# Performance work log

Measured on AMD Instinct MI355X. Metric: run time of the kernel, lower is better.

The kernel has to match this reference:

```python
import jax, jax.numpy as jnp
import numpy as np

B, S, D, V = 2, 2048, 1024, 32000
EPSILON = 5.0


def setup_inputs() -> dict:
    key = jax.random.key(0)
    k1, k2, k3, k4 = jax.random.split(key, 4)
    inputs_embeds = jax.random.normal(k1, (B, S, D), dtype=jnp.float32)
    table = jax.random.normal(k2, (V, D), dtype=jnp.float32)
    # dx-privacy noise: unit-norm Gaussian direction * Gamma(alpha=D, rate=eps*D) scalar sample
    noise_v = jax.random.normal(k3, (B, S, D), dtype=jnp.float32)
    norm = jnp.linalg.norm(noise_v, axis=-1, keepdims=True)
    norm = jnp.where(norm > 0, norm, jnp.ones_like(norm))
    gamma_scale = jax.random.gamma(k4, jnp.float32(D)) / jnp.float32(EPSILON * D)
    noise = gamma_scale * (noise_v / norm)
    return {"inputs_embeds": inputs_embeds, "table": table, "noise": noise}


def reference(inputs_embeds, table, noise):
    # perturb embeddings with precomputed dx-privacy noise (no_grad in original)
    perturbed = inputs_embeds + noise                      # [B,S,D]
    # full similarity matrix vs vocabulary, then nearest-embedding snap
    sims = jnp.einsum('bsd,vd->bsv', perturbed, table)     # [B,S,V]
    max_token = jnp.argmax(sims, axis=-1)                  # [B,S] int
    res = jnp.take(table, max_token, axis=0)               # [B,S,D]
    return res
```

## Files before the change

### kernel.cpp

```cpp
#include <hip/hip_runtime.h>
#include <stdint.h>

#define ROWS 4096
#define DIM 1024
#define VOCAB 32000
#define BM 128
#define BN 128
#define NTILES (VOCAB / BN)
#define NCHUNKS 24
#define SCALE 2048.0f

typedef float floatx4 __attribute__((ext_vector_type(4)));
typedef _Float16 f16x8 __attribute__((ext_vector_type(8)));
typedef _Float16 f16x4 __attribute__((ext_vector_type(4)));

__device__ __forceinline__ void load_lds16(const _Float16* g, _Float16* l) {
    __builtin_amdgcn_global_load_lds(
        (const __attribute__((address_space(1))) uint32_t*)g,
        (__attribute__((address_space(3))) uint32_t*)l, 16, 0, 0);
}

__global__ void init_keys(unsigned long long* __restrict__ keys) {
    int i = blockIdx.x * 256 + threadIdx.x;
    if (i < ROWS) keys[i] = 0ull;
}

__global__ void prep(const float* __restrict__ emb, const float* __restrict__ noi,
                     const float* __restrict__ table,
                     _Float16* __restrict__ Ah, _Float16* __restrict__ Al,
                     _Float16* __restrict__ Bh, _Float16* __restrict__ Bl,
                     unsigned long long* __restrict__ keys) {
    const int bid = blockIdx.x;
    const int ABLK = ROWS * DIM / 8 / 256;
    if (bid < ABLK) {
        if (bid < ROWS / 256) keys[bid * 256 + threadIdx.x] = 0ull;
        size_t i = ((size_t)bid * 256 + threadIdx.x) * 8;
        floatx4 a = *(const floatx4*)(emb + i);
        floatx4 b = *(const floatx4*)(emb + i + 4);
        floatx4 c = *(const floatx4*)(noi + i);
        floatx4 d = *(const floatx4*)(noi + i + 4);
        f16x8 h, l;
#pragma unroll
        for (int j = 0; j < 4; j++) {
            float p = (a[j] + c[j]) * SCALE;
            _Float16 hh = (_Float16)p;
            h[j] = hh; l[j] = (_Float16)(p - (float)hh);
            float q = (b[j] + d[j]) * SCALE;
            _Float16 hq = (_Float16)q;
            h[4 + j] = hq; l[4 + j] = (_Float16)(q - (float)hq);
        }
        *(f16x8*)(Ah + i) = h;
        *(f16x8*)(Al + i) = l;
    } else {
        size_t i = ((size_t)(bid - ABLK) * 256 + threadIdx.x) * 8;
        floatx4 a = *(const floatx4*)(table + i);
        floatx4 b = *(const floatx4*)(table + i + 4);
        f16x8 h, l;
#pragma unroll
        for (int j = 0; j < 4; j++) {
            float p = a[j] * SCALE;
            _Float16 hh = (_Float16)p;
            h[j] = hh; l[j] = (_Float16)(p - (float)hh);
            float q = b[j] * SCALE;
            _Float16 hq = (_Float16)q;
            h[4 + j] = hq; l[4 + j] = (_Float16)(q - (float)hq);
        }
        *(f16x8*)(Bh + i) = h;
        *(f16x8*)(Bl + i) = l;
    }
}

__global__ __launch_bounds__(256, 3) void gemm_argmax_pre(
    const _Float16* __restrict__ Ah, const _Float16* __restrict__ Al,
    const _Float16* __restrict__ Bh, const _Float16* __restrict__ Bl,
    unsigned long long* __restrict__ keys) {
    __shared__ __align__(16) _Float16 sAh[BM * 32];
    __shared__ __align__(16) _Float16 sAl[BM * 32];
    __shared__ __align__(16) _Float16 sBh[BN * 32];
    __shared__ __align__(16) _Float16 sBl[BN * 32];
    __shared__ unsigned long long redk[BM];

    const int tid = threadIdx.x;
    const int w = tid >> 6, lane = tid & 63;
    const int quad = lane >> 4, lq = lane & 15;
    const int rb = blockIdx.x / NCHUNKS, chunk = blockIdx.x % NCHUNKS;
    const int row0 = rb * BM;
    const int wmb = (w & 1) * 4, wnb = (w >> 1) * 4;
    const int wm = wmb * 16, wn = wnb * 16;
    const int tstart = chunk * NTILES / NCHUNKS;
    const int tend = (chunk + 1) * NTILES / NCHUNKS;

    if (tid < BM) redk[tid] = 0ull;

    union PF { f16x8 v; _Float16 s[8]; } fidx, fone;
#pragma unroll
    for (int j = 0; j < 8; j++) { fidx.s[j] = (_Float16)0.0f; fone.s[j] = (_Float16)0.0f; }
    if (quad == 0) { fidx.s[0] = (_Float16)(float)lq; fone.s[0] = (_Float16)1.0f; }
    floatx4 c1 = {0.f, 0.f, 0.f, 0.f}, c2 = {0.f, 0.f, 0.f, 0.f};
    c1 = __builtin_amdgcn_mfma_f32_16x16x32_f16(fidx.v, fone.v, c1, 0, 0, 0);
    c2 = __builtin_amdgcn_mfma_f32_16x16x32_f16(fone.v, fidx.v, c2, 0, 0, 0);
    int m_of[4], n_of[4];
#pragma unroll
    for (int r = 0; r < 4; r++) {
        m_of[r] = (int)(c1[r] + 0.5f);
        n_of[r] = (int)(c2[r] + 0.5f);
    }

    const _Float16* gbase = (w == 0) ? (Ah + (size_t)row0 * DIM)
                        : (w == 1) ? (Al + (size_t)row0 * DIM)
                        : (w == 2) ? Bh : Bl;
    _Float16* ldst = (w == 0) ? sAh : (w == 1) ? sAl : (w == 2) ? sBh : sBl;
    const int piece = (lane & 3) ^ ((lane >> 3) & 3);
    const size_t g_lane = (size_t)(lane >> 2) * DIM + (size_t)piece * 8;
    const int rdo = lq * 32 + (quad ^ ((lq >> 1) & 3)) * 8;
    const bool isB = (w >= 2);

    float rmax[16];
    int ridx[16];
#pragma unroll
    for (int i = 0; i < 16; i++) { rmax[i] = -3.4e38f; ridx[i] = 0; }

    for (int t = tstart; t < tend; ++t) {
        const int n0 = t * BN;
        const _Float16* gsrc = gbase + (isB ? (size_t)t * BN * DIM : 0) + g_lane;
        floatx4 acc[4][4];
#pragma unroll
        for (int mi = 0; mi < 4; mi++)
#pragma unroll
            for (int ni = 0; ni < 4; ni++)
#pragma unroll
                for (int r = 0; r < 4; r++) acc[mi][ni][r] = 0.0f;

        for (int kt = 0; kt < DIM / 32; ++kt) {
            const int k0 = kt * 32;
            __syncthreads();
#pragma unroll
            for (int c = 0; c < 8; c++)
                load_lds16(gsrc + (size_t)(c * 16) * DIM + k0, ldst + c * 512);
            __syncthreads();

            f16x8 ahf[4], alf[4];
#pragma unroll
            for (int i = 0; i < 4; i++) {
                ahf[i] = *(const f16x8*)(&sAh[(wmb + i) * 512 + rdo]);
                alf[i] = *(const f16x8*)(&sAl[(wmb + i) * 512 + rdo]);
            }
#pragma unroll
            for (int ni = 0; ni < 4; ni++) {
                f16x8 bh = *(const f16x8*)(&sBh[(wnb + ni) * 512 + rdo]);
                f16x8 bl = *(const f16x8*)(&sBl[(wnb + ni) * 512 + rdo]);
#pragma unroll
                for (int mi = 0; mi < 4; mi++) {
                    acc[mi][ni] = __builtin_amdgcn_mfma_f32_16x16x32_f16(
                        ahf[mi], bh, acc[mi][ni], 0, 0, 0);
                    acc[mi][ni] = __builtin_amdgcn_mfma_f32_16x16x32_f16(
                        ahf[mi], bl, acc[mi][ni], 0, 0, 0);
                    acc[mi][ni] = __builtin_amdgcn_mfma_f32_16x16x32_f16(
                        alf[mi], bh, acc[mi][ni], 0, 0, 0);
                }
            }
        }
#pragma unroll
        for (int mi = 0; mi < 4; mi++)
#pragma unroll
            for (int ni = 0; ni < 4; ni++)
#pragma unroll
                for (int r = 0; r < 4; r++) {
                    float v = acc[mi][ni][r];
                    int col = n0 + wn + ni * 16 + n_of[r];
                    int s = mi * 4 + r;
                    if (v > rmax[s] || (v == rmax[s] && col < ridx[s])) {
                        rmax[s] = v;
                        ridx[s] = col;
                    }
                }
    }

#pragma unroll
    for (int s = 0; s < 16; ++s) {
        int mi = s >> 2, r = s & 3;
        int rowl = wm + mi * 16 + m_of[r];
        union { float f; uint32_t i; } u;
        u.f = rmax[s];
        uint32_t ord = (u.i & 0x80000000u) ? ~u.i : (u.i | 0x80000000u);
        unsigned long long key =
            ((unsigned long long)ord << 32) | (uint32_t)(~(uint32_t)ridx[s]);
        atomicMax(&redk[rowl], key);
    }
    __syncthreads();
    if (tid < BM) atomicMax(&keys[row0 + tid], redk[tid]);
}

#define BKF 64
#define LDKF 72
#define TILES_PER_WGF 10
#define NCHUNKSF 25

__global__ __launch_bounds__(256, 2) void gemm_argmax_fused(
    const float* __restrict__ emb, const float* __restrict__ noi,
    const float* __restrict__ table, unsigned long long* __restrict__ keys) {
    __shared__ __align__(16) _Float16 Ah[BM * LDKF];
    __shared__ __align__(16) _Float16 Al[BM * LDKF];
    __shared__ __align__(16) _Float16 Bh[BN * LDKF];
    __shared__ __align__(16) _Float16 Bl[BN * LDKF];
    __shared__ unsigned long long redk[BM];

    const int tid = threadIdx.x;
    const int wave = tid >> 6, lane = tid & 63;
    const int quad = lane >> 4, lq = lane & 15;
    const int rb = blockIdx.x / NCHUNKSF, chunk = blockIdx.x % NCHUNKSF;
    const int row0 = rb * BM;
    const int wm = (wave & 1) * 64, wn = (wave >> 1) * 64;

    if (tid < BM) redk[tid] = 0ull;

    union PF { f16x8 v; _Float16 s[8]; } fidx, fone;
#pragma unroll
    for (int j = 0; j < 8; j++) { fidx.s[j] = (_Float16)0.0f; fone.s[j] = (_Float16)0.0f; }
    if (quad == 0) { fidx.s[0] = (_Float16)(float)lq; fone.s[0] = (_Float16)1.0f; }
    floatx4 c1 = {0.f, 0.f, 0.f, 0.f}, c2 = {0.f, 0.f, 0.f, 0.f};
    c1 = __builtin_amdgcn_mfma_f32_16x16x32_f16(fidx.v, fone.v, c1, 0, 0, 0);
    c2 = __builtin_amdgcn_mfma_f32_16x16x32_f16(fone.v, fidx.v, c2, 0, 0, 0);
    int m_of[4], n_of[4];
#pragma unroll
    for (int r = 0; r < 4; r++) {
        m_of[r] = (int)(c1[r] + 0.5f);
        n_of[r] = (int)(c2[r] + 0.5f);
    }

    float rmax[16];
    int ridx[16];
#pragma unroll
    for (int i = 0; i < 16; i++) { rmax[i] = -3.4e38f; ridx[i] = 0; }

    for (int t = 0; t < TILES_PER_WGF; ++t) {
        const int n0 = (chunk * TILES_PER_WGF + t) * BN;
        floatx4 acc[4][4];
#pragma unroll
        for (int mi = 0; mi < 4; mi++)
#pragma unroll
            for (int ni = 0; ni < 4; ni++)
#pragma unroll
                for (int r = 0; r < 4; r++) acc[mi][ni][r] = 0.0f;

        for (int kt = 0; kt < DIM / BKF; ++kt) {
            const int k0 = kt * BKF;
            __syncthreads();
#pragma unroll
            for (int i = 0; i < 8; i++) {
                int c = i * 256 + tid;
                int r = c >> 4, q = c & 15;
                floatx4 e = *(const floatx4*)(emb + (size_t)(row0 + r) * DIM + k0 + q * 4);
                floatx4 n = *(const floatx4*)(noi + (size_t)(row0 + r) * DIM + k0 + q * 4);
                floatx4 b = *(const floatx4*)(table + (size_t)(n0 + r) * DIM + k0 + q * 4);
                f16x4 ah, al, bh, bl;
#pragma unroll
                for (int j = 0; j < 4; j++) {
                    float pa = (e[j] + n[j]) * SCALE;
                    _Float16 h = (_Float16)pa;
                    ah[j] = h;
                    al[j] = (_Float16)(pa - (float)h);
                    float pb = b[j] * SCALE;
                    _Float16 hb = (_Float16)pb;
                    bh[j] = hb;
                    bl[j] = (_Float16)(pb - (float)hb);
                }
                *(f16x4*)(Ah + r * LDKF + q * 4) = ah;
                *(f16x4*)(Al + r * LDKF + q * 4) = al;
                *(f16x4*)(Bh + r * LDKF + q * 4) = bh;
                *(f16x4*)(Bl + r * LDKF + q * 4) = bl;
            }
            __syncthreads();
#pragma unroll
            for (int ks = 0; ks < BKF; ks += 32) {
                f16x8 bhf[4], blf[4], ahf[4], alf[4];
#pragma unroll
                for (int i = 0; i < 4; i++) {
                    bhf[i] = *(const f16x8*)(Bh + (wn + i * 16 + lq) * LDKF + ks + quad * 8);
                    blf[i] = *(const f16x8*)(Bl + (wn + i * 16 + lq) * LDKF + ks + quad * 8);
                    ahf[i] = *(const f16x8*)(Ah + (wm + i * 16 + lq) * LDKF + ks + quad * 8);
                    alf[i] = *(const f16x8*)(Al + (wm + i * 16 + lq) * LDKF + ks + quad * 8);
                }
#pragma unroll
                for (int mi = 0; mi < 4; mi++)
#pragma unroll
                    for (int ni = 0; ni < 4; ni++) {
                        acc[mi][ni] = __builtin_amdgcn_mfma_f32_16x16x32_f16(
                            ahf[mi], bhf[ni], acc[mi][ni], 0, 0, 0);
                        acc[mi][ni] = __builtin_amdgcn_mfma_f32_16x16x32_f16(
                            ahf[mi], blf[ni], acc[mi][ni], 0, 0, 0);
                        acc[mi][ni] = __builtin_amdgcn_mfma_f32_16x16x32_f16(
                            alf[mi], bhf[ni], acc[mi][ni], 0, 0, 0);
                    }
            }
        }
#pragma unroll
        for (int mi = 0; mi < 4; mi++)
#pragma unroll
            for (int ni = 0; ni < 4; ni++)
#pragma unroll
                for (int r = 0; r < 4; r++) {
                    float v = acc[mi][ni][r];
                    int col = n0 + wn + ni * 16 + n_of[r];
                    int s = mi * 4 + r;
                    if (v > rmax[s] || (v == rmax[s] && col < ridx[s])) {
                        rmax[s] = v;
                        ridx[s] = col;
                    }
                }
    }

#pragma unroll
    for (int s = 0; s < 16; ++s) {
        int mi = s >> 2, r = s & 3;
        int rowl = wm + mi * 16 + m_of[r];
        union { float f; uint32_t i; } u;
        u.f = rmax[s];
        uint32_t ord = (u.i & 0x80000000u) ? ~u.i : (u.i | 0x80000000u);
        unsigned long long key =
            ((unsigned long long)ord << 32) | (uint32_t)(~(uint32_t)ridx[s]);
        atomicMax(&redk[rowl], key);
    }
    __syncthreads();
    if (tid < BM) atomicMax(&keys[row0 + tid], redk[tid]);
}

__global__ void gather_kernel(const unsigned long long* __restrict__ keys,
                              const float* __restrict__ table,
                              float* __restrict__ out) {
    int row = blockIdx.x;
    unsigned long long key = keys[row];
    uint32_t ix = ~(uint32_t)(key & 0xFFFFFFFFull);
    const floatx4* src = (const floatx4*)(table + (size_t)ix * DIM);
    floatx4* dst = (floatx4*)(out + (size_t)row * DIM);
    dst[threadIdx.x] = src[threadIdx.x];
}

extern "C" void kernel_launch(void* const* d_in, const int* in_sizes, int n_in,
                              void* d_out, int out_size, void* d_ws, size_t ws_size,
                              hipStream_t stream) {
    (void)in_sizes; (void)n_in; (void)out_size;
    const float* emb = (const float*)d_in[0];
    const float* table = (const float*)d_in[1];
    const float* noi = (const float*)d_in[2];
    float* out = (float*)d_out;

    uint8_t* ws = (uint8_t*)d_ws;
    unsigned long long* keys = (unsigned long long*)ws;
    const size_t keysB = (size_t)ROWS * 8;
    const size_t aB = (size_t)ROWS * DIM * 2;
    const size_t bB = (size_t)VOCAB * DIM * 2;
    const size_t need = keysB + 2 * aB + 2 * bB;

    if (ws_size >= need) {
        _Float16* Ah = (_Float16*)(ws + keysB);
        _Float16* Al = (_Float16*)(ws + keysB + aB);
        _Float16* Bh = (_Float16*)(ws + keysB + 2 * aB);
        _Float16* Bl = (_Float16*)(ws + keysB + 2 * aB + bB);
        const int ablk = ROWS * DIM / 8 / 256;
        const int bblk = VOCAB * DIM / 8 / 256;
        prep<<<ablk + bblk, 256, 0, stream>>>(emb, noi, table, Ah, Al, Bh, Bl, keys);
        gemm_argmax_pre<<<(ROWS / BM) * NCHUNKS, 256, 0, stream>>>(Ah, Al, Bh, Bl, keys);
    } else {
        init_keys<<<ROWS / 256, 256, 0, stream>>>(keys);
        gemm_argmax_fused<<<(ROWS / BM) * NCHUNKSF, 256, 0, stream>>>(emb, noi, table, keys);
    }
    gather_kernel<<<ROWS, 256, 0, stream>>>(keys, table, out);
}
```

Measured before the change: 1.044 ms.

## Shrink pre-split GEMM tiles to 64x64 and double-buffer LDS loads

```diff
diff --git a/kernel.cpp b/kernel.cpp
--- a/kernel.cpp
+++ b/kernel.cpp
@@ -6,8 +6,10 @@
 #define VOCAB 32000
 #define BM 128
 #define BN 128
-#define NTILES (VOCAB / BN)
-#define NCHUNKS 24
+#define BMP 64
+#define BNP 64
+#define NTILESP (VOCAB / BNP)
+#define NCHUNKSP 12
 #define SCALE 2048.0f
 
 typedef float floatx4 __attribute__((ext_vector_type(4)));
@@ -74,23 +76,23 @@
     const _Float16* __restrict__ Ah, const _Float16* __restrict__ Al,
     const _Float16* __restrict__ Bh, const _Float16* __restrict__ Bl,
     unsigned long long* __restrict__ keys) {
-    __shared__ __align__(16) _Float16 sAh[BM * 32];
-    __shared__ __align__(16) _Float16 sAl[BM * 32];
-    __shared__ __align__(16) _Float16 sBh[BN * 32];
-    __shared__ __align__(16) _Float16 sBl[BN * 32];
-    __shared__ unsigned long long redk[BM];
+    __shared__ __align__(16) _Float16 sAh[2][BMP * 32];
+    __shared__ __align__(16) _Float16 sAl[2][BMP * 32];
+    __shared__ __align__(16) _Float16 sBh[2][BNP * 32];
+    __shared__ __align__(16) _Float16 sBl[2][BNP * 32];
+    __shared__ unsigned long long redk[BMP];
 
     const int tid = threadIdx.x;
     const int w = tid >> 6, lane = tid & 63;
     const int quad = lane >> 4, lq = lane & 15;
-    const int rb = blockIdx.x / NCHUNKS, chunk = blockIdx.x % NCHUNKS;
-    const int row0 = rb * BM;
-    const int wmb = (w & 1) * 4, wnb = (w >> 1) * 4;
+    const int rb = blockIdx.x / NCHUNKSP, chunk = blockIdx.x % NCHUNKSP;
+    const int row0 = rb * BMP;
+    const int wmb = (w & 1) * 2, wnb = (w >> 1) * 2;
     const int wm = wmb * 16, wn = wnb * 16;
-    const int tstart = chunk * NTILES / NCHUNKS;
-    const int tend = (chunk + 1) * NTILES / NCHUNKS;
-
-    if (tid < BM) redk[tid] = 0ull;
+    const int tstart = chunk * NTILESP / NCHUNKSP;
+    const int tend = (chunk + 1) * NTILESP / NCHUNKSP;
+
+    if (tid < BMP) redk[tid] = 0ull;
 
     union PF { f16x8 v; _Float16 s[8]; } fidx, fone;
 #pragma unroll
@@ -109,48 +111,65 @@
     const _Float16* gbase = (w == 0) ? (Ah + (size_t)row0 * DIM)
                         : (w == 1) ? (Al + (size_t)row0 * DIM)
                         : (w == 2) ? Bh : Bl;
-    _Float16* ldst = (w == 0) ? sAh : (w == 1) ? sAl : (w == 2) ? sBh : sBl;
+    _Float16* lbase = (w == 0) ? &sAh[0][0] : (w == 1) ? &sAl[0][0]
+                    : (w == 2) ? &sBh[0][0] : &sBl[0][0];
     const int piece = (lane & 3) ^ ((lane >> 3) & 3);
     const size_t g_lane = (size_t)(lane >> 2) * DIM + (size_t)piece * 8;
     const int rdo = lq * 32 + (quad ^ ((lq >> 1) & 3)) * 8;
     const bool isB = (w >= 2);
 
-    float rmax[16];
-    int ridx[16];
-#pragma unroll
-    for (int i = 0; i < 16; i++) { rmax[i] = -3.4e38f; ridx[i] = 0; }
+    float rmax[8];
+    int ridx[8];
+#pragma unroll
+    for (int i = 0; i < 8; i++) { rmax[i] = -3.4e38f; ridx[i] = 0; }
+
+#define STAGE(buf, tt, kk)                                                     \
+    do {                                                                       \
+        const _Float16* gs_ = gbase + (isB ? (size_t)(tt) * BNP * DIM : 0)     \
+                              + (size_t)(kk) * 32 + g_lane;                    \
+        _Float16* ld_ = lbase + (buf) * (BMP * 32);                            \
+        _Pragma("unroll")                                                      \
+        for (int c_ = 0; c_ < 4; c_++)                                         \
+            load_lds16(gs_ + (size_t)(c_ * 16) * DIM, ld_ + c_ * 512);         \
+    } while (0)
+
+    int cur = 0;
+    STAGE(0, tstart, 0);
 
     for (int t = tstart; t < tend; ++t) {
-        const int n0 = t * BN;
-        const _Float16* gsrc = gbase + (isB ? (size_t)t * BN * DIM : 0) + g_lane;
-        floatx4 acc[4][4];
-#pragma unroll
-        for (int mi = 0; mi < 4; mi++)
-#pragma unroll
-            for (int ni = 0; ni < 4; ni++)
+        const int n0 = t * BNP;
+        floatx4 acc[2][2];
+#pragma unroll
+        for (int mi = 0; mi < 2; mi++)
+#pragma unroll
+            for (int ni = 0; ni < 2; ni++)
 #pragma unroll
                 for (int r = 0; r < 4; r++) acc[mi][ni][r] = 0.0f;
 
         for (int kt = 0; kt < DIM / 32; ++kt) {
-            const int k0 = kt * 32;
-            __syncthreads();
-#pragma unroll
-            for (int c = 0; c < 8; c++)
-                load_lds16(gsrc + (size_t)(c * 16) * DIM + k0, ldst + c * 512);
-            __syncthreads();
-
-            f16x8 ahf[4], alf[4];
-#pragma unroll
-            for (int i = 0; i < 4; i++) {
-                ahf[i] = *(const f16x8*)(&sAh[(wmb + i) * 512 + rdo]);
-                alf[i] = *(const f16x8*)(&sAl[(wmb + i) * 512 + rdo]);
-            }
-#pragma unroll
-            for (int ni = 0; ni < 4; ni++) {
-                f16x8 bh = *(const f16x8*)(&sBh[(wnb + ni) * 512 + rdo]);
-                f16x8 bl = *(const f16x8*)(&sBl[(wnb + ni) * 512 + rdo]);
-#pragma unroll
-                for (int mi = 0; mi < 4; mi++) {
+            int nt = t, nk = kt + 1;
+            if (nk == DIM / 32) { nk = 0; ++nt; }
+            if (nt < tend) {
+                STAGE(cur ^ 1, nt, nk);
+                asm volatile("s_waitcnt vmcnt(4)" ::: "memory");
+            } else {
+                asm volatile("s_waitcnt vmcnt(0)" ::: "memory");
+            }
+            __builtin_amdgcn_s_barrier();
+
+            __builtin_amdgcn_s_setprio(1);
+            f16x8 ahf[2], alf[2];
+#pragma unroll
+            for (int i = 0; i < 2; i++) {
+                ahf[i] = *(const f16x8*)(&sAh[cur][(wmb + i) * 512 + rdo]);
+                alf[i] = *(const f16x8*)(&sAl[cur][(wmb + i) * 512 + rdo]);
+            }
+#pragma unroll
+            for (int ni = 0; ni < 2; ni++) {
+                f16x8 bh = *(const f16x8*)(&sBh[cur][(wnb + ni) * 512 + rdo]);
+                f16x8 bl = *(const f16x8*)(&sBl[cur][(wnb + ni) * 512 + rdo]);
+#pragma unroll
+                for (int mi = 0; mi < 2; mi++) {
                     acc[mi][ni] = __builtin_amdgcn_mfma_f32_16x16x32_f16(
                         ahf[mi], bh, acc[mi][ni], 0, 0, 0);
                     acc[mi][ni] = __builtin_amdgcn_mfma_f32_16x16x32_f16(
@@ -158,6 +177,146 @@
                     acc[mi][ni] = __builtin_amdgcn_mfma_f32_16x16x32_f16(
                         alf[mi], bh, acc[mi][ni], 0, 0, 0);
                 }
+            }
+            __builtin_amdgcn_s_setprio(0);
+
+            asm volatile("s_waitcnt lgkmcnt(0)" ::: "memory");
+            __builtin_amdgcn_s_barrier();
+            cur ^= 1;
+        }
+#pragma unroll
+        for (int mi = 0; mi < 2; mi++)
+#pragma unroll
+            for (int ni = 0; ni < 2; ni++)
+#pragma unroll
+                for (int r = 0; r < 4; r++) {
+                    float v = acc[mi][ni][r];
+                    int col = n0 + wn + ni * 16 + n_of[r];
+                    int s = mi * 4 + r;
+                    if (v > rmax[s] || (v == rmax[s] && col < ridx[s])) {
+                        rmax[s] = v;
+                        ridx[s] = col;
+                    }
+                }
+    }
+#undef STAGE
+
+#pragma unroll
+    for (int s = 0; s < 8; ++s) {
+        int mi = s >> 2, r = s & 3;
+        int rowl = wm + mi * 16 + m_of[r];
+        union { float f; uint32_t i; } u;
+        u.f = rmax[s];
+        uint32_t ord = (u.i & 0x80000000u) ? ~u.i : (u.i | 0x80000000u);
+        unsigned long long key =
+            ((unsigned long long)ord << 32) | (uint32_t)(~(uint32_t)ridx[s]);
+        atomicMax(&redk[rowl], key);
+    }
+    __syncthreads();
+    if (tid < BMP) atomicMax(&keys[row0 + tid], redk[tid]);
+}
+
+#define BKF 64
+#define LDKF 72
+#define TILES_PER_WGF 10
+#define NCHUNKSF 25
+
+__global__ __launch_bounds__(256, 2) void gemm_argmax_fused(
+    const float* __restrict__ emb, const float* __restrict__ noi,
+    const float* __restrict__ table, unsigned long long* __restrict__ keys) {
+    __shared__ __align__(16) _Float16 Ah[BM * LDKF];
+    __shared__ __align__(16) _Float16 Al[BM * LDKF];
+    __shared__ __align__(16) _Float16 Bh[BN * LDKF];
+    __shared__ __align__(16) _Float16 Bl[BN * LDKF];
+    __shared__ unsigned long long redk[BM];
+
+    const int tid = threadIdx.x;
+    const int wave = tid >> 6, lane = tid & 63;
+    const int quad = lane >> 4, lq = lane & 15;
+    const int rb = blockIdx.x / NCHUNKSF, chunk = blockIdx.x % NCHUNKSF;
+    const int row0 = rb * BM;
+    const int wm = (wave & 1) * 64, wn = (wave >> 1) * 64;
+
+    if (tid < BM) redk[tid] = 0ull;
+
+    union PF { f16x8 v; _Float16 s[8]; } fidx, fone;
+#pragma unroll
+    for (int j = 0; j < 8; j++) { fidx.s[j] = (_Float16)0.0f; fone.s[j] = (_Float16)0.0f; }
+    if (quad == 0) { fidx.s[0] = (_Float16)(float)lq; fone.s[0] = (_Float16)1.0f; }
+    floatx4 c1 = {0.f, 0.f, 0.f, 0.f}, c2 = {0.f, 0.f, 0.f, 0.f};
+    c1 = __builtin_amdgcn_mfma_f32_16x16x32_f16(fidx.v, fone.v, c1, 0, 0, 0);
+    c2 = __builtin_amdgcn_mfma_f32_16x16x32_f16(fone.v, fidx.v, c2, 0, 0, 0);
+    int m_of[4], n_of[4];
+#pragma unroll
+    for (int r = 0; r < 4; r++) {
+        m_of[r] = (int)(c1[r] + 0.5f);
+        n_of[r] = (int)(c2[r] + 0.5f);
+    }
+
+    float rmax[16];
+    int ridx[16];
+#pragma unroll
+    for (int i = 0; i < 16; i++) { rmax[i] = -3.4e38f; ridx[i] = 0; }
+
+    for (int t = 0; t < TILES_PER_WGF; ++t) {
+        const int n0 = (chunk * TILES_PER_WGF + t) * BN;
+        floatx4 acc[4][4];
+#pragma unroll
+        for (int mi = 0; mi < 4; mi++)
+#pragma unroll
+            for (int ni = 0; ni < 4; ni++)
+#pragma unroll
+                for (int r = 0; r < 4; r++) acc[mi][ni][r] = 0.0f;
+
+        for (int kt = 0; kt < DIM / BKF; ++kt) {
+            const int k0 = kt * BKF;
+            __syncthreads();
+#pragma unroll
+            for (int i = 0; i < 8; i++) {
+                int c = i * 256 + tid;
+                int r = c >> 4, q = c & 15;
+                floatx4 e = *(const floatx4*)(emb + (size_t)(row0 + r) * DIM + k0 + q * 4);
+                floatx4 n = *(const floatx4*)(noi + (size_t)(row0 + r) * DIM + k0 + q * 4);
+                floatx4 b = *(const floatx4*)(table + (size_t)(n0 + r) * DIM + k0 + q * 4);
+                f16x4 ah, al, bh, bl;
+#pragma unroll
+                for (int j = 0; j < 4; j++) {
+                    float pa = (e[j] + n[j]) * SCALE;
+                    _Float16 h = (_Float16)pa;
+                    ah[j] = h;
+                    al[j] = (_Float16)(pa - (float)h);
+                    float pb = b[j] * SCALE;
+                    _Float16 hb = (_Float16)pb;
+                    bh[j] = hb;
+                    bl[j] = (_Float16)(pb - (float)hb);
+                }
+                *(f16x4*)(Ah + r * LDKF + q * 4) = ah;
+                *(f16x4*)(Al + r * LDKF + q * 4) = al;
+                *(f16x4*)(Bh + r * LDKF + q * 4) = bh;
+                *(f16x4*)(Bl + r * LDKF + q * 4) = bl;
+            }
+            __syncthreads();
+#pragma unroll
+            for (int ks = 0; ks < BKF; ks += 32) {
+                f16x8 bhf[4], blf[4], ahf[4], alf[4];
+#pragma unroll
+                for (int i = 0; i < 4; i++) {
+                    bhf[i] = *(const f16x8*)(Bh + (wn + i * 16 + lq) * LDKF + ks + quad * 8);
+                    blf[i] = *(const f16x8*)(Bl + (wn + i * 16 + lq) * LDKF + ks + quad * 8);
+                    ahf[i] = *(const f16x8*)(Ah + (wm + i * 16 + lq) * LDKF + ks + quad * 8);
+                    alf[i] = *(const f16x8*)(Al + (wm + i * 16 + lq) * LDKF + ks + quad * 8);
+                }
+#pragma unroll
+                for (int mi = 0; mi < 4; mi++)
+#pragma unroll
+                    for (int ni = 0; ni < 4; ni++) {
+                        acc[mi][ni] = __builtin_amdgcn_mfma_f32_16x16x32_f16(
+                            ahf[mi], bhf[ni], acc[mi][ni], 0, 0, 0);
+                        acc[mi][ni] = __builtin_amdgcn_mfma_f32_16x16x32_f16(
+                            ahf[mi], blf[ni], acc[mi][ni], 0, 0, 0);
+                        acc[mi][ni] = __builtin_amdgcn_mfma_f32_16x16x32_f16(
+                            alf[mi], bhf[ni], acc[mi][ni], 0, 0, 0);
+                    }
             }
         }
 #pragma unroll
@@ -191,140 +350,6 @@
     if (tid < BM) atomicMax(&keys[row0 + tid], redk[tid]);
 }
 
-#define BKF 64
-#define LDKF 72
-#define TILES_PER_WGF 10
-#define NCHUNKSF 25
-
-__global__ __launch_bounds__(256, 2) void gemm_argmax_fused(
-    const float* __restrict__ emb, const float* __restrict__ noi,
-    const float* __restrict__ table, unsigned long long* __restrict__ keys) {
-    __shared__ __align__(16) _Float16 Ah[BM * LDKF];
-    __shared__ __align__(16) _Float16 Al[BM * LDKF];
-    __shared__ __align__(16) _Float16 Bh[BN * LDKF];
-    __shared__ __align__(16) _Float16 Bl[BN * LDKF];
-    __shared__ unsigned long long redk[BM];
-
-    const int tid = threadIdx.x;
-    const int wave = tid >> 6, lane = tid & 63;
-    const int quad = lane >> 4, lq = lane & 15;
-    const int rb = blockIdx.x / NCHUNKSF, chunk = blockIdx.x % NCHUNKSF;
-    const int row0 = rb * BM;
-    const int wm = (wave & 1) * 64, wn = (wave >> 1) * 64;
-
-    if (tid < BM) redk[tid] = 0ull;
-
-    union PF { f16x8 v; _Float16 s[8]; } fidx, fone;
-#pragma unroll
-    for (int j = 0; j < 8; j++) { fidx.s[j] = (_Float16)0.0f; fone.s[j] = (_Float16)0.0f; }
-    if (quad == 0) { fidx.s[0] = (_Float16)(float)lq; fone.s[0] = (_Float16)1.0f; }
-    floatx4 c1 = {0.f, 0.f, 0.f, 0.f}, c2 = {0.f, 0.f, 0.f, 0.f};
-    c1 = __builtin_amdgcn_mfma_f32_16x16x32_f16(fidx.v, fone.v, c1, 0, 0, 0);
-    c2 = __builtin_amdgcn_mfma_f32_16x16x32_f16(fone.v, fidx.v, c2, 0, 0, 0);
-    int m_of[4], n_of[4];
-#pragma unroll
-    for (int r = 0; r < 4; r++) {
-        m_of[r] = (int)(c1[r] + 0.5f);
-        n_of[r] = (int)(c2[r] + 0.5f);
-    }
-
-    float rmax[16];
-    int ridx[16];
-#pragma unroll
-    for (int i = 0; i < 16; i++) { rmax[i] = -3.4e38f; ridx[i] = 0; }
-
-    for (int t = 0; t < TILES_PER_WGF; ++t) {
-        const int n0 = (chunk * TILES_PER_WGF + t) * BN;
-        floatx4 acc[4][4];
-#pragma unroll
-        for (int mi = 0; mi < 4; mi++)
-#pragma unroll
-            for (int ni = 0; ni < 4; ni++)
-#pragma unroll
-                for (int r = 0; r < 4; r++) acc[mi][ni][r] = 0.0f;
-
-        for (int kt = 0; kt < DIM / BKF; ++kt) {
-            const int k0 = kt * BKF;
-            __syncthreads();
-#pragma unroll
-            for (int i = 0; i < 8; i++) {
-                int c = i * 256 + tid;
-                int r = c >> 4, q = c & 15;
-                floatx4 e = *(const floatx4*)(emb + (size_t)(row0 + r) * DIM + k0 + q * 4);
-                floatx4 n = *(const floatx4*)(noi + (size_t)(row0 + r) * DIM + k0 + q * 4);
-                floatx4 b = *(const floatx4*)(table + (size_t)(n0 + r) * DIM + k0 + q * 4);
-                f16x4 ah, al, bh, bl;
-#pragma unroll
-                for (int j = 0; j < 4; j++) {
-                    float pa = (e[j] + n[j]) * SCALE;
-                    _Float16 h = (_Float16)pa;
-                    ah[j] = h;
-                    al[j] = (_Float16)(pa - (float)h);
-                    float pb = b[j] * SCALE;
-                    _Float16 hb = (_Float16)pb;
-                    bh[j] = hb;
-                    bl[j] = (_Float16)(pb - (float)hb);
-                }
-                *(f16x4*)(Ah + r * LDKF + q * 4) = ah;
-                *(f16x4*)(Al + r * LDKF + q * 4) = al;
-                *(f16x4*)(Bh + r * LDKF + q * 4) = bh;
-                *(f16x4*)(Bl + r * LDKF + q * 4) = bl;
-            }
-            __syncthreads();
-#pragma unroll
-            for (int ks = 0; ks < BKF; ks += 32) {
-                f16x8 bhf[4], blf[4], ahf[4], alf[4];
-#pragma unroll
-                for (int i = 0; i < 4; i++) {
-                    bhf[i] = *(const f16x8*)(Bh + (wn + i * 16 + lq) * LDKF + ks + quad * 8);
-                    blf[i] = *(const f16x8*)(Bl + (wn + i * 16 + lq) * LDKF + ks + quad * 8);
-                    ahf[i] = *(const f16x8*)(Ah + (wm + i * 16 + lq) * LDKF + ks + quad * 8);
-                    alf[i] = *(const f16x8*)(Al + (wm + i * 16 + lq) * LDKF + ks + quad * 8);
-                }
-#pragma unroll
-                for (int mi = 0; mi < 4; mi++)
-#pragma unroll
-                    for (int ni = 0; ni < 4; ni++) {
-                        acc[mi][ni] = __builtin_amdgcn_mfma_f32_16x16x32_f16(
-                            ahf[mi], bhf[ni], acc[mi][ni], 0, 0, 0);
-                        acc[mi][ni] = __builtin_amdgcn_mfma_f32_16x16x32_f16(
-                            ahf[mi], blf[ni], acc[mi][ni], 0, 0, 0);
-                        acc[mi][ni] = __builtin_amdgcn_mfma_f32_16x16x32_f16(
-                            alf[mi], bhf[ni], acc[mi][ni], 0, 0, 0);
-                    }
-            }
-        }
-#pragma unroll
-        for (int mi = 0; mi < 4; mi++)
-#pragma unroll
-            for (int ni = 0; ni < 4; ni++)
-#pragma unroll
-                for (int r = 0; r < 4; r++) {
-                    float v = acc[mi][ni][r];
-                    int col = n0 + wn + ni * 16 + n_of[r];
-                    int s = mi * 4 + r;
-                    if (v > rmax[s] || (v == rmax[s] && col < ridx[s])) {
-                        rmax[s] = v;
-                        ridx[s] = col;
-                    }
-                }
-    }
-
-#pragma unroll
-    for (int s = 0; s < 16; ++s) {
-        int mi = s >> 2, r = s & 3;
-        int rowl = wm + mi * 16 + m_of[r];
-        union { float f; uint32_t i; } u;
-        u.f = rmax[s];
-        uint32_t ord = (u.i & 0x80000000u) ? ~u.i : (u.i | 0x80000000u);
-        unsigned long long key =
-            ((unsigned long long)ord << 32) | (uint32_t)(~(uint32_t)ridx[s]);
-        atomicMax(&redk[rowl], key);
-    }
-    __syncthreads();
-    if (tid < BM) atomicMax(&keys[row0 + tid], redk[tid]);
-}
-
 __global__ void gather_kernel(const unsigned long long* __restrict__ keys,
                               const float* __restrict__ table,
                               float* __restrict__ out) {
@@ -360,7 +385,7 @@
         const int ablk = ROWS * DIM / 8 / 256;
         const int bblk = VOCAB * DIM / 8 / 256;
         prep<<<ablk + bblk, 256, 0, stream>>>(emb, noi, table, Ah, Al, Bh, Bl, keys);
-        gemm_argmax_pre<<<(ROWS / BM) * NCHUNKS, 256, 0, stream>>>(Ah, Al, Bh, Bl, keys);
+        gemm_argmax_pre<<<(ROWS / BMP) * NCHUNKSP, 256, 0, stream>>>(Ah, Al, Bh, Bl, keys);
     } else {
         init_keys<<<ROWS / 256, 256, 0, stream>>>(keys);
         gemm_argmax_fused<<<(ROWS / BM) * NCHUNKSF, 256, 0, stream>>>(emb, noi, table, keys);
```

After: 1.595 ms. 1.53x slower.
